# Kernel tuning notes

Measured on AMD Instinct MI355X. Metric: run time of the kernel, lower is better.

## Reference

```python
import jax, jax.numpy as jnp
import numpy as np

N = 100000
IN_DIM = 128
OUT_DIM = 128
E = 3200000


def setup_inputs() -> dict:
    key = jax.random.key(0)
    k1, k2, k3, k4, k5 = jax.random.split(key, 5)
    x = jax.random.normal(k1, (N, IN_DIM), dtype=jnp.float32)
    src = jax.random.randint(k2, (E,), 0, N)
    dst = jax.random.randint(k3, (E,), 0, N)
    edge_index = jnp.stack([src, dst], axis=0)  # (2, E) int
    # Linear(2*in_dim, out_dim): torch stores weight as (out, in)
    bound = 1.0 / np.sqrt(2 * IN_DIM)
    W = jax.random.uniform(k4, (OUT_DIM, 2 * IN_DIM), minval=-bound, maxval=bound, dtype=jnp.float32)
    b = jax.random.uniform(k5, (OUT_DIM,), minval=-bound, maxval=bound, dtype=jnp.float32)
    return {"x": x, "edge_index": edge_index, "W": W, "b": b}


def reference(x, edge_index, W, b):
    # x: (N, d), edge_index: (2, E)
    n = x.shape[0]
    src, dst = edge_index[0], edge_index[1]
    # scatter-add of source features into target buckets (mean aggregation)
    agg = jax.ops.segment_sum(x[src], dst, num_segments=n)          # (N, d)
    count = jax.ops.segment_sum(jnp.ones((src.shape[0],), x.dtype), dst, num_segments=n)
    count = jnp.maximum(count, 1.0)[:, None]                         # (N, 1)
    neigh_mean = agg / count
    combined = jnp.concatenate([x, neigh_mean], axis=1)              # (N, 2d)
    return combined @ W.T + b
```

## Files before the change

### kernel.cpp

```cpp
#include <hip/hip_runtime.h>

typedef unsigned int u32;
typedef unsigned short u16;
typedef unsigned char u8;
typedef _Float16 half8 __attribute__((ext_vector_type(8)));
typedef float f32x4 __attribute__((ext_vector_type(4)));
typedef float f32x2 __attribute__((ext_vector_type(2)));

__global__ __launch_bounds__(256) void pre_k(const float* __restrict__ x, u16* __restrict__ xh,
                                             u32* __restrict__ xq,
                                             const float* __restrict__ W, u16* __restrict__ wh,
                                             const int* __restrict__ dst, int E,
                                             u32* __restrict__ bktTotal, int N, int nbkt,
                                             int nba, int nbx) {
  int b = blockIdx.x, tid = threadIdx.x;
  if (b < nba) {
    __shared__ u32 h[512];
    for (int t = tid; t < 512; t += 256) h[t] = 0u;
    __syncthreads();
    int base = b * 8192;
    for (int it = 0; it < 32; it++) {
      int i = base + it * 256 + tid;
      if (i < E) atomicAdd(&h[(u32)dst[i] >> 8], 1u);
    }
    __syncthreads();
    for (int t = tid; t < nbkt; t += 256) {
      u32 c = h[t];
      if (c) atomicAdd(&bktTotal[t], c);
    }
  } else if (b < nba + nbx) {
    int i = (b - nba) * 256 + tid;
    if (i < N * 32) {
      const float4 v = *(const float4*)(x + (size_t)i * 4);
      u32 p0 = __builtin_bit_cast(u32, __builtin_amdgcn_cvt_pkrtz(v.x, v.y));
      u32 p1 = __builtin_bit_cast(u32, __builtin_amdgcn_cvt_pkrtz(v.z, v.w));
      *(uint2*)(xh + (size_t)i * 4) = uint2{p0, p1};
      u32 q = 0;
      q = __builtin_amdgcn_cvt_pk_fp8_f32(v.x, v.y, q, false);
      q = __builtin_amdgcn_cvt_pk_fp8_f32(v.z, v.w, q, true);
      xq[i] = q;
    }
  } else {
    int i = (b - nba - nbx) * 256 + tid;
    if (i < 8192) {
      const float4 v = *(const float4*)(W + (size_t)i * 4);
      u32 p0 = __builtin_bit_cast(u32, __builtin_amdgcn_cvt_pkrtz(v.x, v.y));
      u32 p1 = __builtin_bit_cast(u32, __builtin_amdgcn_cvt_pkrtz(v.z, v.w));
      *(uint2*)(wh + (size_t)i * 4) = uint2{p0, p1};
    }
  }
}

__global__ __launch_bounds__(512) void bscan_k(const u32* __restrict__ bktTotal, int nbkt,
                                               int E, int N, u32* __restrict__ start,
                                               u32* __restrict__ cursor, u32* __restrict__ offsets) {
  __shared__ u32 s[512];
  int t = threadIdx.x;
  u32 v = (t < nbkt) ? bktTotal[t] : 0u;
  s[t] = v;
  __syncthreads();
  for (int off = 1; off < 512; off <<= 1) {
    u32 x = (t >= off) ? s[t - off] : 0u;
    __syncthreads();
    s[t] += x;
    __syncthreads();
  }
  u32 excl = s[t] - v;
  if (t < nbkt) { start[t] = excl; cursor[t] = excl; }
  if (t == nbkt - 1) start[nbkt] = excl + v;
  if (t == 0) offsets[N] = (u32)E;
}

__global__ __launch_bounds__(256) void part_k(const int* __restrict__ src, const int* __restrict__ dst,
                                              int E, u32* __restrict__ cursor,
                                              u32* __restrict__ packed, int nbkt) {
  __shared__ u32 h[512];
  for (int t = threadIdx.x; t < 512; t += 256) h[t] = 0u;
  __syncthreads();
  int base = blockIdx.x * 8192;
  for (int it = 0; it < 32; it++) {
    int i = base + it * 256 + threadIdx.x;
    if (i < E) atomicAdd(&h[(u32)dst[i] >> 8], 1u);
  }
  __syncthreads();
  for (int t = threadIdx.x; t < nbkt; t += 256) {
    u32 c = h[t];
    h[t] = c ? atomicAdd(&cursor[t], c) : 0u;
  }
  __syncthreads();
  for (int it = 0; it < 32; it++) {
    int i = base + it * 256 + threadIdx.x;
    if (i < E) {
      u32 d = (u32)dst[i];
      u32 pos = atomicAdd(&h[d >> 8], 1u);
      packed[pos] = (u32)src[i] | ((d & 255u) << 24);
    }
  }
}

__global__ __launch_bounds__(256) void bucket_k(const u32* __restrict__ packed,
                                                const u32* __restrict__ start, int N,
                                                u32* __restrict__ offsets, int* __restrict__ ssrc,
                                                u8* __restrict__ nodeperm) {
  __shared__ u32 cnt[256];
  __shared__ u32 scn[256];
  __shared__ u32 cur[256];
  int b = blockIdx.x, t = threadIdx.x;
  u32 lo = start[b], hi = start[b + 1];
  cnt[t] = 0u;
  __syncthreads();
  for (u32 j = lo + t; j < hi; j += 256) atomicAdd(&cnt[packed[j] >> 24], 1u);
  __syncthreads();
  u32 v = cnt[t];
  scn[t] = v;
  __syncthreads();
  for (int off = 1; off < 256; off <<= 1) {
    u32 x = (t >= off) ? scn[t - off] : 0u;
    __syncthreads();
    scn[t] += x;
    __syncthreads();
  }
  u32 base = lo + scn[t] - v;
  int node = b * 256 + t;
  if (node < N) offsets[node] = base;
  cur[t] = base;
  __syncthreads();
  for (u32 j = lo + t; j < hi; j += 256) {
    u32 w = packed[j];
    u32 pos = atomicAdd(&cur[w >> 24], 1u);
    ssrc[pos] = (int)(w & 0xFFFFFFu);
  }
  {
    int g = t >> 5, l = t & 31;
    u32 mykey = cnt[t] * 256u + (u32)l;
    const u32* cg = &cnt[g * 32];
    u32 rank = 0;
#pragma unroll 8
    for (int l2 = 0; l2 < 32; l2++) {
      u32 k2 = cg[l2] * 256u + (u32)l2;
      rank += (k2 < mykey) ? 1u : 0u;
    }
    nodeperm[(size_t)b * 256 + g * 32 + rank] = (u8)l;
  }
}

#define DECV(vv, A0, A1, A2, A3) { f32x2 p;                              \
    p = __builtin_amdgcn_cvt_pk_f32_fp8((vv).x, false); A0 += p;         \
    p = __builtin_amdgcn_cvt_pk_f32_fp8((vv).x, true);  A1 += p;         \
    p = __builtin_amdgcn_cvt_pk_f32_fp8((vv).y, false); A2 += p;         \
    p = __builtin_amdgcn_cvt_pk_f32_fp8((vv).y, true);  A3 += p; }

__global__ __launch_bounds__(256) void fuse_k(const int* __restrict__ ssrc,
                                              const u32* __restrict__ offsets,
                                              const u32* __restrict__ xq,
                                              const u16* __restrict__ xh,
                                              const u16* __restrict__ wh,
                                              const float* __restrict__ bias,
                                              const u8* __restrict__ nodeperm,
                                              float* __restrict__ out, int N) {
  __shared__ u16 mlds[32][136];
  int wv = threadIdx.x >> 6, lane = threadIdx.x & 63;
  int sub = lane >> 4, cl = lane & 15;
  int nbase = blockIdx.x * 32;

  for (int r = 0; r < 2; r++) {
    int ln = nodeperm[(size_t)nbase + r * 16 + wv * 4 + sub];
    int node = nbase + ln;
    f32x2 A0{0.f,0.f}, A1{0.f,0.f}, A2{0.f,0.f}, A3{0.f,0.f};
    u32 deg = 0;
    if (node < N) {
      u32 s0 = offsets[node], s1 = offsets[node + 1];
      deg = s1 - s0;
      u32 j = s0;
      u32 nq = deg >> 2;
      if (nq) {
        uint4 iA = *(const uint4*)(ssrc + j);
        for (u32 q = 1; q < nq; q++) {
          uint4 iN = *(const uint4*)(ssrc + j + 4);
          uint2 v0 = *(const uint2*)(xq + ((size_t)iA.x << 5) + (cl << 1));
          uint2 v1 = *(const uint2*)(xq + ((size_t)iA.y << 5) + (cl << 1));
          uint2 v2 = *(const uint2*)(xq + ((size_t)iA.z << 5) + (cl << 1));
          uint2 v3 = *(const uint2*)(xq + ((size_t)iA.w << 5) + (cl << 1));
          DECV(v0, A0, A1, A2, A3) DECV(v1, A0, A1, A2, A3)
          DECV(v2, A0, A1, A2, A3) DECV(v3, A0, A1, A2, A3)
          iA = iN; j += 4;
        }
        {
          uint2 v0 = *(const uint2*)(xq + ((size_t)iA.x << 5) + (cl << 1));
          uint2 v1 = *(const uint2*)(xq + ((size_t)iA.y << 5) + (cl << 1));
          uint2 v2 = *(const uint2*)(xq + ((size_t)iA.z << 5) + (cl << 1));
          uint2 v3 = *(const uint2*)(xq + ((size_t)iA.w << 5) + (cl << 1));
          DECV(v0, A0, A1, A2, A3) DECV(v1, A0, A1, A2, A3)
          DECV(v2, A0, A1, A2, A3) DECV(v3, A0, A1, A2, A3)
          j += 4;
        }
      }
      for (; j < s1; j++) {
        int e = ssrc[j];
        uint2 v = *(const uint2*)(xq + ((size_t)e << 5) + (cl << 1));
        DECV(v, A0, A1, A2, A3)
      }
    }
    float inv = 1.0f / (float)(deg ? deg : 1u);
    u32 o0 = __builtin_bit_cast(u32, __builtin_amdgcn_cvt_pkrtz(A0.x * inv, A0.y * inv));
    u32 o1 = __builtin_bit_cast(u32, __builtin_amdgcn_cvt_pkrtz(A1.x * inv, A1.y * inv));
    u32 o2 = __builtin_bit_cast(u32, __builtin_amdgcn_cvt_pkrtz(A2.x * inv, A2.y * inv));
    u32 o3 = __builtin_bit_cast(u32, __builtin_amdgcn_cvt_pkrtz(A3.x * inv, A3.y * inv));
    *(uint4*)&mlds[ln][cl * 8] = uint4{o0, o1, o2, o3};
  }
  __syncthreads();

  int la = lane & 15, lb = lane >> 4;
  int strip = wv & 1, ch = wv >> 1;
  int rbase = nbase + strip * 16;
  half8 a[8];
  const u16* ab = xh + ((size_t)(rbase + la) << 7) + lb * 8;
#pragma unroll
  for (int kb = 0; kb < 4; kb++) a[kb] = *(const half8*)(ab + kb * 32);
#pragma unroll
  for (int kb = 0; kb < 4; kb++)
    a[4 + kb] = *(const half8*)(&mlds[strip * 16 + la][kb * 32 + lb * 8]);

#pragma unroll
  for (int c = 0; c < 4; c++) {
    int ct = ch * 4 + c;
    f32x4 acc = { 0.f, 0.f, 0.f, 0.f };
    const u16* bbase = wh + ((size_t)(ct * 16 + la) << 8) + lb * 8;
#pragma unroll
    for (int kb = 0; kb < 8; kb++) {
      half8 b = *(const half8*)(bbase + kb * 32);
      acc = __builtin_amdgcn_mfma_f32_16x16x32_f16(a[kb], b, acc, 0, 0, 0);
    }
    float bc = bias[ct * 16 + la];
#pragma unroll
    for (int jj = 0; jj < 4; jj++) {
      int rr = rbase + lb * 4 + jj;
      if (rr < N) out[((size_t)rr << 7) + ct * 16 + la] = acc[jj] + bc;
    }
  }
}

extern "C" void kernel_launch(void* const* d_in, const int* in_sizes, int n_in,
                              void* d_out, int out_size, void* d_ws, size_t ws_size,
                              hipStream_t stream) {
  const float* x    = (const float*)d_in[0];
  const int*   ei   = (const int*)d_in[1];
  const float* W    = (const float*)d_in[2];
  const float* bias = (const float*)d_in[3];
  const int N = in_sizes[0] / 128;
  const int E = in_sizes[1] / 2;
  const int nbkt = (N + 255) >> 8;
  const int* src = ei;
  const int* dst = ei + E;
  float* out = (float*)d_out;

  u32* packed   = (u32*)d_out;
  u32* bktTotal = packed + E;
  u32* start    = bktTotal + nbkt;
  u32* cursor   = start + nbkt + 1;

  char* ws = (char*)d_ws;
  u32* offsets = (u32*)ws;
  size_t off = ((size_t)(N + 1) * 4 + 255) & ~(size_t)255;
  int* ssrc = (int*)(ws + off);
  off += (size_t)E * 4;
  off = (off + 255) & ~(size_t)255;
  u16* xh = (u16*)(ws + off);
  off += (size_t)N * 128 * 2;
  off = (off + 255) & ~(size_t)255;
  u32* xq = (u32*)(ws + off);
  off += (size_t)N * 128;
  off = (off + 255) & ~(size_t)255;
  u16* wh = (u16*)(ws + off);
  off += (size_t)128 * 256 * 2;
  off = (off + 255) & ~(size_t)255;
  u8* nodeperm = (u8*)(ws + off);

  const int nbx = (N * 32 + 255) / 256;
  const int nba = (E + 8191) / 8192;
  hipMemsetAsync(bktTotal, 0, (size_t)nbkt * 4, stream);
  pre_k<<<nba + nbx + 32, 256, 0, stream>>>(x, xh, xq, W, wh, dst, E, bktTotal, N, nbkt, nba, nbx);
  bscan_k<<<1, 512, 0, stream>>>(bktTotal, nbkt, E, N, start, cursor, offsets);
  part_k<<<nba, 256, 0, stream>>>(src, dst, E, cursor, packed, nbkt);
  bucket_k<<<nbkt, 256, 0, stream>>>(packed, start, N, offsets, ssrc, nodeperm);
  fuse_k<<<(N + 31) / 32, 256, 0, stream>>>(ssrc, offsets, xq, xh, wh, bias, nodeperm, out, N);
}
```

Before: 208.1 us.

## Stage block edge indices in LDS and double-buffer neighbor gathers

Each block now cooperatively loads its contiguous range of sorted source indices (up to a fixed capacity) into shared memory, and per-node loops read indices from LDS instead of global memory. The gather loop is restructured to keep two groups of four neighbor-row loads in flight, consuming one while the next is issued. This aims to hide gather latency and remove the dependent global index loads from the critical path. It costs extra LDS, a block-wide barrier, and more registers, which may reduce occupancy.

```diff
diff --git a/kernel.cpp b/kernel.cpp
--- a/kernel.cpp
+++ b/kernel.cpp
@@ -6,6 +6,8 @@
 typedef _Float16 half8 __attribute__((ext_vector_type(8)));
 typedef float f32x4 __attribute__((ext_vector_type(4)));
 typedef float f32x2 __attribute__((ext_vector_type(2)));
+
+#define CAP 1536
 
 __global__ __launch_bounds__(256) void pre_k(const float* __restrict__ x, u16* __restrict__ xh,
                                              u32* __restrict__ xq,
@@ -144,11 +146,24 @@
   }
 }
 
-#define DECV(vv, A0, A1, A2, A3) { f32x2 p;                              \
+#define DECV(vv) { f32x2 p;                                              \
     p = __builtin_amdgcn_cvt_pk_f32_fp8((vv).x, false); A0 += p;         \
     p = __builtin_amdgcn_cvt_pk_f32_fp8((vv).x, true);  A1 += p;         \
     p = __builtin_amdgcn_cvt_pk_f32_fp8((vv).y, false); A2 += p;         \
     p = __builtin_amdgcn_cvt_pk_f32_fp8((vv).y, true);  A3 += p; }
+
+#define LOADQ(V0, V1, V2, V3, I) { \
+    V0 = *(const uint2*)(xq + ((size_t)(I).x << 5) + (cl << 1)); \
+    V1 = *(const uint2*)(xq + ((size_t)(I).y << 5) + (cl << 1)); \
+    V2 = *(const uint2*)(xq + ((size_t)(I).z << 5) + (cl << 1)); \
+    V3 = *(const uint2*)(xq + ((size_t)(I).w << 5) + (cl << 1)); }
+
+#define CONSQ(V0, V1, V2, V3) { DECV(V0) DECV(V1) DECV(V2) DECV(V3) }
+
+#define IDX4(O, DST) { if (inl) { int o_ = (int)(O); \
+      DST.x = (u32)eidx[o_]; DST.y = (u32)eidx[o_ + 1]; \
+      DST.z = (u32)eidx[o_ + 2]; DST.w = (u32)eidx[o_ + 3]; } \
+    else DST = *(const uint4*)((const u32*)ssrc + S0 + (O)); }
 
 __global__ __launch_bounds__(256) void fuse_k(const int* __restrict__ ssrc,
                                               const u32* __restrict__ offsets,
@@ -158,10 +173,24 @@
                                               const float* __restrict__ bias,
                                               const u8* __restrict__ nodeperm,
                                               float* __restrict__ out, int N) {
+  __shared__ int eidx[CAP];
   __shared__ u16 mlds[32][136];
   int wv = threadIdx.x >> 6, lane = threadIdx.x & 63;
   int sub = lane >> 4, cl = lane & 15;
+  int tid = threadIdx.x;
   int nbase = blockIdx.x * 32;
+
+  u32 S0 = offsets[nbase];
+  u32 S1 = offsets[nbase + 32 <= N ? nbase + 32 : N];
+  int cntE = (int)(S1 - S0);
+  int stg = cntE < CAP ? cntE : CAP;
+  for (int i = tid * 4; i + 3 < stg; i += 1024)
+    *(uint4*)&eidx[i] = *(const uint4*)(ssrc + S0 + i);
+  {
+    int base4 = stg & ~3;
+    if (tid < (stg & 3)) eidx[base4 + tid] = ssrc[S0 + base4 + tid];
+  }
+  __syncthreads();
 
   for (int r = 0; r < 2; r++) {
     int ln = nodeperm[(size_t)nbase + r * 16 + wv * 4 + sub];
@@ -171,34 +200,54 @@
     if (node < N) {
       u32 s0 = offsets[node], s1 = offsets[node + 1];
       deg = s1 - s0;
-      u32 j = s0;
+      const bool inl = ((s1 - S0) <= (u32)CAP);
+      u32 lb0 = s0 - S0;
       u32 nq = deg >> 2;
-      if (nq) {
-        uint4 iA = *(const uint4*)(ssrc + j);
-        for (u32 q = 1; q < nq; q++) {
-          uint4 iN = *(const uint4*)(ssrc + j + 4);
-          uint2 v0 = *(const uint2*)(xq + ((size_t)iA.x << 5) + (cl << 1));
-          uint2 v1 = *(const uint2*)(xq + ((size_t)iA.y << 5) + (cl << 1));
-          uint2 v2 = *(const uint2*)(xq + ((size_t)iA.z << 5) + (cl << 1));
-          uint2 v3 = *(const uint2*)(xq + ((size_t)iA.w << 5) + (cl << 1));
-          DECV(v0, A0, A1, A2, A3) DECV(v1, A0, A1, A2, A3)
-          DECV(v2, A0, A1, A2, A3) DECV(v3, A0, A1, A2, A3)
-          iA = iN; j += 4;
+      uint2 vA0, vA1, vA2, vA3, vB0, vB1, vB2, vB3;
+      u32 j;
+      if (nq >= 2) {
+        uint4 iA, iB;
+        IDX4(lb0, iA)
+        IDX4(lb0 + 4, iB)
+        LOADQ(vA0, vA1, vA2, vA3, iA)
+        LOADQ(vB0, vB1, vB2, vB3, iB)
+        u32 q = 2;
+        for (; q + 1 < nq; q += 2) {
+          uint4 i1, i2;
+          IDX4(lb0 + q * 4, i1)
+          IDX4(lb0 + q * 4 + 4, i2)
+          CONSQ(vA0, vA1, vA2, vA3)
+          LOADQ(vA0, vA1, vA2, vA3, i1)
+          CONSQ(vB0, vB1, vB2, vB3)
+          LOADQ(vB0, vB1, vB2, vB3, i2)
         }
-        {
-          uint2 v0 = *(const uint2*)(xq + ((size_t)iA.x << 5) + (cl << 1));
-          uint2 v1 = *(const uint2*)(xq + ((size_t)iA.y << 5) + (cl << 1));
-          uint2 v2 = *(const uint2*)(xq + ((size_t)iA.z << 5) + (cl << 1));
-          uint2 v3 = *(const uint2*)(xq + ((size_t)iA.w << 5) + (cl << 1));
-          DECV(v0, A0, A1, A2, A3) DECV(v1, A0, A1, A2, A3)
-          DECV(v2, A0, A1, A2, A3) DECV(v3, A0, A1, A2, A3)
-          j += 4;
+        if (q < nq) {
+          uint4 i1;
+          IDX4(lb0 + q * 4, i1)
+          CONSQ(vA0, vA1, vA2, vA3)
+          LOADQ(vA0, vA1, vA2, vA3, i1)
+          CONSQ(vB0, vB1, vB2, vB3)
+          CONSQ(vA0, vA1, vA2, vA3)
+          q++;
+        } else {
+          CONSQ(vA0, vA1, vA2, vA3)
+          CONSQ(vB0, vB1, vB2, vB3)
         }
+        j = s0 + nq * 4u;
+      } else if (nq == 1) {
+        uint4 iA;
+        IDX4(lb0, iA)
+        LOADQ(vA0, vA1, vA2, vA3, iA)
+        CONSQ(vA0, vA1, vA2, vA3)
+        j = s0 + 4u;
+      } else {
+        j = s0;
       }
       for (; j < s1; j++) {
-        int e = ssrc[j];
+        u32 o = j - S0;
+        int e = inl ? eidx[o] : ssrc[j];
         uint2 v = *(const uint2*)(xq + ((size_t)e << 5) + (cl << 1));
-        DECV(v, A0, A1, A2, A3)
+        DECV(v)
       }
     }
     float inv = 1.0f / (float)(deg ? deg : 1u);
```

Measured after the change: 209.1 us. About the same (+0.5%).

## Fuse per-node bucket sort into gather kernel using 64-node buckets in LDS

Applied to the files above, without the earlier changes.

Drops the separate bucket_k pass. Edges are partitioned into 64-node buckets, and each fuse_k block sorts its bucket's edges by destination node in shared memory, in tiles of up to CAP entries, before gathering. This removes the global ssrc/offsets/nodeperm writes and reads and one kernel launch. It also enlarges the partition blocks and moves packed into the workspace. The cost is larger LDS use per block, which lowers occupancy, plus extra LDS sort work inside the gather kernel. Buckets with more edges than CAP fall back to a multi-tile path without degree-sorted scheduling.

```diff
diff --git a/kernel.cpp b/kernel.cpp
--- a/kernel.cpp
+++ b/kernel.cpp
@@ -6,6 +6,11 @@
 typedef _Float16 half8 __attribute__((ext_vector_type(8)));
 typedef float f32x4 __attribute__((ext_vector_type(4)));
 typedef float f32x2 __attribute__((ext_vector_type(2)));
+
+#define BK 64
+#define CAP 3072
+#define EB 32768
+#define HSZ 1568
 
 __global__ __launch_bounds__(256) void pre_k(const float* __restrict__ x, u16* __restrict__ xh,
                                              u32* __restrict__ xq,
@@ -15,13 +20,13 @@
                                              int nba, int nbx) {
   int b = blockIdx.x, tid = threadIdx.x;
   if (b < nba) {
-    __shared__ u32 h[512];
-    for (int t = tid; t < 512; t += 256) h[t] = 0u;
-    __syncthreads();
-    int base = b * 8192;
-    for (int it = 0; it < 32; it++) {
+    __shared__ u32 h[HSZ];
+    for (int t = tid; t < HSZ; t += 256) h[t] = 0u;
+    __syncthreads();
+    int base = b * EB;
+    for (int it = 0; it < EB / 256; it++) {
       int i = base + it * 256 + tid;
-      if (i < E) atomicAdd(&h[(u32)dst[i] >> 8], 1u);
+      if (i < E) atomicAdd(&h[(u32)dst[i] >> 6], 1u);
     }
     __syncthreads();
     for (int t = tid; t < nbkt; t += 256) {
@@ -51,36 +56,38 @@
   }
 }
 
-__global__ __launch_bounds__(512) void bscan_k(const u32* __restrict__ bktTotal, int nbkt,
-                                               int E, int N, u32* __restrict__ start,
-                                               u32* __restrict__ cursor, u32* __restrict__ offsets) {
-  __shared__ u32 s[512];
+__global__ __launch_bounds__(1024) void bscan_k(const u32* __restrict__ bktTotal, int nbkt,
+                                                u32* __restrict__ start, u32* __restrict__ cursor) {
+  __shared__ u32 s[1024];
   int t = threadIdx.x;
-  u32 v = (t < nbkt) ? bktTotal[t] : 0u;
-  s[t] = v;
-  __syncthreads();
-  for (int off = 1; off < 512; off <<= 1) {
+  int i0 = t * 2, i1 = t * 2 + 1;
+  u32 a = (i0 < nbkt) ? bktTotal[i0] : 0u;
+  u32 b = (i1 < nbkt) ? bktTotal[i1] : 0u;
+  u32 sum = a + b;
+  s[t] = sum;
+  __syncthreads();
+  for (int off = 1; off < 1024; off <<= 1) {
     u32 x = (t >= off) ? s[t - off] : 0u;
     __syncthreads();
     s[t] += x;
     __syncthreads();
   }
-  u32 excl = s[t] - v;
-  if (t < nbkt) { start[t] = excl; cursor[t] = excl; }
-  if (t == nbkt - 1) start[nbkt] = excl + v;
-  if (t == 0) offsets[N] = (u32)E;
+  u32 excl = s[t] - sum;
+  if (i0 < nbkt) { start[i0] = excl; cursor[i0] = excl; }
+  if (i1 < nbkt) { start[i1] = excl + a; cursor[i1] = excl + a; }
+  if (t == 1023) start[nbkt] = s[1023];
 }
 
 __global__ __launch_bounds__(256) void part_k(const int* __restrict__ src, const int* __restrict__ dst,
                                               int E, u32* __restrict__ cursor,
                                               u32* __restrict__ packed, int nbkt) {
-  __shared__ u32 h[512];
-  for (int t = threadIdx.x; t < 512; t += 256) h[t] = 0u;
-  __syncthreads();
-  int base = blockIdx.x * 8192;
-  for (int it = 0; it < 32; it++) {
+  __shared__ u32 h[HSZ];
+  for (int t = threadIdx.x; t < HSZ; t += 256) h[t] = 0u;
+  __syncthreads();
+  int base = blockIdx.x * EB;
+  for (int it = 0; it < EB / 256; it++) {
     int i = base + it * 256 + threadIdx.x;
-    if (i < E) atomicAdd(&h[(u32)dst[i] >> 8], 1u);
+    if (i < E) atomicAdd(&h[(u32)dst[i] >> 6], 1u);
   }
   __syncthreads();
   for (int t = threadIdx.x; t < nbkt; t += 256) {
@@ -88,142 +95,145 @@
     h[t] = c ? atomicAdd(&cursor[t], c) : 0u;
   }
   __syncthreads();
-  for (int it = 0; it < 32; it++) {
+  for (int it = 0; it < EB / 256; it++) {
     int i = base + it * 256 + threadIdx.x;
     if (i < E) {
       u32 d = (u32)dst[i];
-      u32 pos = atomicAdd(&h[d >> 8], 1u);
-      packed[pos] = (u32)src[i] | ((d & 255u) << 24);
-    }
-  }
-}
-
-__global__ __launch_bounds__(256) void bucket_k(const u32* __restrict__ packed,
-                                                const u32* __restrict__ start, int N,
-                                                u32* __restrict__ offsets, int* __restrict__ ssrc,
-                                                u8* __restrict__ nodeperm) {
-  __shared__ u32 cnt[256];
-  __shared__ u32 scn[256];
-  __shared__ u32 cur[256];
-  int b = blockIdx.x, t = threadIdx.x;
-  u32 lo = start[b], hi = start[b + 1];
-  cnt[t] = 0u;
-  __syncthreads();
-  for (u32 j = lo + t; j < hi; j += 256) atomicAdd(&cnt[packed[j] >> 24], 1u);
-  __syncthreads();
-  u32 v = cnt[t];
-  scn[t] = v;
-  __syncthreads();
-  for (int off = 1; off < 256; off <<= 1) {
-    u32 x = (t >= off) ? scn[t - off] : 0u;
-    __syncthreads();
-    scn[t] += x;
-    __syncthreads();
-  }
-  u32 base = lo + scn[t] - v;
-  int node = b * 256 + t;
-  if (node < N) offsets[node] = base;
-  cur[t] = base;
-  __syncthreads();
-  for (u32 j = lo + t; j < hi; j += 256) {
-    u32 w = packed[j];
-    u32 pos = atomicAdd(&cur[w >> 24], 1u);
-    ssrc[pos] = (int)(w & 0xFFFFFFu);
-  }
-  {
-    int g = t >> 5, l = t & 31;
-    u32 mykey = cnt[t] * 256u + (u32)l;
-    const u32* cg = &cnt[g * 32];
-    u32 rank = 0;
-#pragma unroll 8
-    for (int l2 = 0; l2 < 32; l2++) {
-      u32 k2 = cg[l2] * 256u + (u32)l2;
-      rank += (k2 < mykey) ? 1u : 0u;
-    }
-    nodeperm[(size_t)b * 256 + g * 32 + rank] = (u8)l;
-  }
-}
-
-#define DECV(vv, A0, A1, A2, A3) { f32x2 p;                              \
-    p = __builtin_amdgcn_cvt_pk_f32_fp8((vv).x, false); A0 += p;         \
-    p = __builtin_amdgcn_cvt_pk_f32_fp8((vv).x, true);  A1 += p;         \
-    p = __builtin_amdgcn_cvt_pk_f32_fp8((vv).y, false); A2 += p;         \
-    p = __builtin_amdgcn_cvt_pk_f32_fp8((vv).y, true);  A3 += p; }
-
-__global__ __launch_bounds__(256) void fuse_k(const int* __restrict__ ssrc,
-                                              const u32* __restrict__ offsets,
+      u32 pos = atomicAdd(&h[d >> 6], 1u);
+      packed[pos] = (u32)src[i] | ((d & 63u) << 24);
+    }
+  }
+}
+
+#define DECQ(vv, B0, B1, B2, B3) { f32x2 p;                              \
+    p = __builtin_amdgcn_cvt_pk_f32_fp8((vv).x, false); B0 += p;         \
+    p = __builtin_amdgcn_cvt_pk_f32_fp8((vv).x, true);  B1 += p;         \
+    p = __builtin_amdgcn_cvt_pk_f32_fp8((vv).y, false); B2 += p;         \
+    p = __builtin_amdgcn_cvt_pk_f32_fp8((vv).y, true);  B3 += p; }
+
+#define GATHER(LN, B0, B1, B2, B3, DG) {                                          \
+    u32 sb = o64[LN]; u32 c = c64[LN]; DG += c;                                   \
+    u32 nq = c >> 2;                                                              \
+    if (nq) {                                                                     \
+      const int* ep = &eidx[sb];                                                  \
+      uint4 iA; iA.x=(u32)ep[0]; iA.y=(u32)ep[1]; iA.z=(u32)ep[2]; iA.w=(u32)ep[3]; \
+      for (u32 qq = 1; qq < nq; qq++) {                                           \
+        const int* en = &eidx[sb + qq * 4u];                                      \
+        uint4 iN; iN.x=(u32)en[0]; iN.y=(u32)en[1]; iN.z=(u32)en[2]; iN.w=(u32)en[3]; \
+        uint2 v0 = *(const uint2*)(xq + ((size_t)iA.x << 5) + (cl << 1));         \
+        uint2 v1 = *(const uint2*)(xq + ((size_t)iA.y << 5) + (cl << 1));         \
+        uint2 v2 = *(const uint2*)(xq + ((size_t)iA.z << 5) + (cl << 1));         \
+        uint2 v3 = *(const uint2*)(xq + ((size_t)iA.w << 5) + (cl << 1));         \
+        DECQ(v0, B0, B1, B2, B3) DECQ(v1, B0, B1, B2, B3)                         \
+        DECQ(v2, B0, B1, B2, B3) DECQ(v3, B0, B1, B2, B3)                         \
+        iA = iN;                                                                  \
+      }                                                                           \
+      {                                                                           \
+        uint2 v0 = *(const uint2*)(xq + ((size_t)iA.x << 5) + (cl << 1));         \
+        uint2 v1 = *(const uint2*)(xq + ((size_t)iA.y << 5) + (cl << 1));         \
+        uint2 v2 = *(const uint2*)(xq + ((size_t)iA.z << 5) + (cl << 1));         \
+        uint2 v3 = *(const uint2*)(xq + ((size_t)iA.w << 5) + (cl << 1));         \
+        DECQ(v0, B0, B1, B2, B3) DECQ(v1, B0, B1, B2, B3)                         \
+        DECQ(v2, B0, B1, B2, B3) DECQ(v3, B0, B1, B2, B3)                         \
+      }                                                                           \
+    }                                                                             \
+    for (u32 j = nq * 4u; j < c; j++) {                                           \
+      u32 e = (u32)eidx[sb + j];                                                  \
+      uint2 v = *(const uint2*)(xq + ((size_t)e << 5) + (cl << 1));               \
+      DECQ(v, B0, B1, B2, B3)                                                     \
+    } }
+
+#define WRMEAN(LN, B0, B1, B2, B3, DG) {                                          \
+    float inv = 1.0f / (float)((DG) ? (DG) : 1u);                                 \
+    u32 q0 = __builtin_bit_cast(u32, __builtin_amdgcn_cvt_pkrtz(B0.x*inv, B0.y*inv)); \
+    u32 q1 = __builtin_bit_cast(u32, __builtin_amdgcn_cvt_pkrtz(B1.x*inv, B1.y*inv)); \
+    u32 q2 = __builtin_bit_cast(u32, __builtin_amdgcn_cvt_pkrtz(B2.x*inv, B2.y*inv)); \
+    u32 q3 = __builtin_bit_cast(u32, __builtin_amdgcn_cvt_pkrtz(B3.x*inv, B3.y*inv)); \
+    *(uint4*)&mlds[LN][cl * 8] = uint4{q0, q1, q2, q3}; }
+
+__global__ __launch_bounds__(256) void fuse_k(const u32* __restrict__ packed,
+                                              const u32* __restrict__ start,
                                               const u32* __restrict__ xq,
                                               const u16* __restrict__ xh,
                                               const u16* __restrict__ wh,
                                               const float* __restrict__ bias,
-                                              const u8* __restrict__ nodeperm,
                                               float* __restrict__ out, int N) {
-  __shared__ u16 mlds[32][136];
-  int wv = threadIdx.x >> 6, lane = threadIdx.x & 63;
+  __shared__ int eidx[CAP];
+  __shared__ u16 mlds[64][136];
+  __shared__ u32 c64[64], o64[64], cur64[64], perm[64];
+  int tid = threadIdx.x, wv = tid >> 6, lane = tid & 63;
   int sub = lane >> 4, cl = lane & 15;
-  int nbase = blockIdx.x * 32;
-
-  for (int r = 0; r < 2; r++) {
-    int ln = nodeperm[(size_t)nbase + r * 16 + wv * 4 + sub];
-    int node = nbase + ln;
-    f32x2 A0{0.f,0.f}, A1{0.f,0.f}, A2{0.f,0.f}, A3{0.f,0.f};
-    u32 deg = 0;
-    if (node < N) {
-      u32 s0 = offsets[node], s1 = offsets[node + 1];
-      deg = s1 - s0;
-      u32 j = s0;
-      u32 nq = deg >> 2;
-      if (nq) {
-        uint4 iA = *(const uint4*)(ssrc + j);
-        for (u32 q = 1; q < nq; q++) {
-          uint4 iN = *(const uint4*)(ssrc + j + 4);
-          uint2 v0 = *(const uint2*)(xq + ((size_t)iA.x << 5) + (cl << 1));
-          uint2 v1 = *(const uint2*)(xq + ((size_t)iA.y << 5) + (cl << 1));
-          uint2 v2 = *(const uint2*)(xq + ((size_t)iA.z << 5) + (cl << 1));
-          uint2 v3 = *(const uint2*)(xq + ((size_t)iA.w << 5) + (cl << 1));
-          DECV(v0, A0, A1, A2, A3) DECV(v1, A0, A1, A2, A3)
-          DECV(v2, A0, A1, A2, A3) DECV(v3, A0, A1, A2, A3)
-          iA = iN; j += 4;
-        }
-        {
-          uint2 v0 = *(const uint2*)(xq + ((size_t)iA.x << 5) + (cl << 1));
-          uint2 v1 = *(const uint2*)(xq + ((size_t)iA.y << 5) + (cl << 1));
-          uint2 v2 = *(const uint2*)(xq + ((size_t)iA.z << 5) + (cl << 1));
-          uint2 v3 = *(const uint2*)(xq + ((size_t)iA.w << 5) + (cl << 1));
-          DECV(v0, A0, A1, A2, A3) DECV(v1, A0, A1, A2, A3)
-          DECV(v2, A0, A1, A2, A3) DECV(v3, A0, A1, A2, A3)
-          j += 4;
-        }
+  int nbase = blockIdx.x * BK;
+  u32 lo = start[blockIdx.x], hi = start[blockIdx.x + 1];
+  u32 cnt = hi - lo;
+  int ntiles = (int)((cnt + (CAP - 1)) / CAP);
+  bool single = (ntiles <= 1);
+
+  f32x2 A00{0,0},A01{0,0},A02{0,0},A03{0,0};
+  f32x2 A10{0,0},A11{0,0},A12{0,0},A13{0,0};
+  f32x2 A20{0,0},A21{0,0},A22{0,0},A23{0,0};
+  f32x2 A30{0,0},A31{0,0},A32{0,0},A33{0,0};
+  u32 dg0 = 0, dg1 = 0, dg2 = 0, dg3 = 0;
+  int rb = wv * 4 + sub;
+  int ln0 = rb, ln1 = 16 + rb, ln2 = 32 + rb, ln3 = 48 + rb;
+
+  for (int t = 0; t < ntiles; t++) {
+    u32 tb = lo + (u32)t * CAP;
+    u32 rem = hi - tb;
+    int tsz = (int)(rem < (u32)CAP ? rem : (u32)CAP);
+    if (tid < 64) c64[tid] = 0u;
+    __syncthreads();
+    for (int i = tid; i < tsz; i += 256) atomicAdd(&c64[packed[tb + i] >> 24], 1u);
+    __syncthreads();
+    if (tid < 64) {
+      u32 mc = c64[tid];
+      u32 mykey = mc * 64u + (u32)tid;
+      u32 o = 0, rank = 0;
+      for (int l = 0; l < 64; l++) {
+        u32 cv = c64[l];
+        if (l < tid) o += cv;
+        u32 k2 = cv * 64u + (u32)l;
+        rank += (k2 < mykey) ? 1u : 0u;
       }
-      for (; j < s1; j++) {
-        int e = ssrc[j];
-        uint2 v = *(const uint2*)(xq + ((size_t)e << 5) + (cl << 1));
-        DECV(v, A0, A1, A2, A3)
-      }
-    }
-    float inv = 1.0f / (float)(deg ? deg : 1u);
-    u32 o0 = __builtin_bit_cast(u32, __builtin_amdgcn_cvt_pkrtz(A0.x * inv, A0.y * inv));
-    u32 o1 = __builtin_bit_cast(u32, __builtin_amdgcn_cvt_pkrtz(A1.x * inv, A1.y * inv));
-    u32 o2 = __builtin_bit_cast(u32, __builtin_amdgcn_cvt_pkrtz(A2.x * inv, A2.y * inv));
-    u32 o3 = __builtin_bit_cast(u32, __builtin_amdgcn_cvt_pkrtz(A3.x * inv, A3.y * inv));
-    *(uint4*)&mlds[ln][cl * 8] = uint4{o0, o1, o2, o3};
-  }
+      o64[tid] = o; cur64[tid] = o;
+      perm[rank] = (u32)tid;
+    }
+    __syncthreads();
+    for (int i = tid; i < tsz; i += 256) {
+      u32 w = packed[tb + i];
+      u32 pos = atomicAdd(&cur64[w >> 24], 1u);
+      eidx[pos] = (int)(w & 0xFFFFFFu);
+    }
+    __syncthreads();
+    if (single) {
+      ln0 = (int)perm[rb]; ln1 = (int)perm[16 + rb];
+      ln2 = (int)perm[32 + rb]; ln3 = (int)perm[48 + rb];
+    }
+    GATHER(ln0, A00, A01, A02, A03, dg0)
+    GATHER(ln1, A10, A11, A12, A13, dg1)
+    GATHER(ln2, A20, A21, A22, A23, dg2)
+    GATHER(ln3, A30, A31, A32, A33, dg3)
+    __syncthreads();
+  }
+
+  WRMEAN(ln0, A00, A01, A02, A03, dg0)
+  WRMEAN(ln1, A10, A11, A12, A13, dg1)
+  WRMEAN(ln2, A20, A21, A22, A23, dg2)
+  WRMEAN(ln3, A30, A31, A32, A33, dg3)
   __syncthreads();
 
   int la = lane & 15, lb = lane >> 4;
-  int strip = wv & 1, ch = wv >> 1;
-  int rbase = nbase + strip * 16;
+  int wbase = nbase + wv * 16;
   half8 a[8];
-  const u16* ab = xh + ((size_t)(rbase + la) << 7) + lb * 8;
+  const u16* ab = xh + ((size_t)(wbase + la) << 7) + lb * 8;
 #pragma unroll
   for (int kb = 0; kb < 4; kb++) a[kb] = *(const half8*)(ab + kb * 32);
 #pragma unroll
   for (int kb = 0; kb < 4; kb++)
-    a[4 + kb] = *(const half8*)(&mlds[strip * 16 + la][kb * 32 + lb * 8]);
-
-#pragma unroll
-  for (int c = 0; c < 4; c++) {
-    int ct = ch * 4 + c;
+    a[4 + kb] = *(const half8*)(&mlds[wv * 16 + la][kb * 32 + lb * 8]);
+
+#pragma unroll
+  for (int ct = 0; ct < 8; ct++) {
     f32x4 acc = { 0.f, 0.f, 0.f, 0.f };
     const u16* bbase = wh + ((size_t)(ct * 16 + la) << 8) + lb * 8;
 #pragma unroll
@@ -234,7 +244,7 @@
     float bc = bias[ct * 16 + la];
 #pragma unroll
     for (int jj = 0; jj < 4; jj++) {
-      int rr = rbase + lb * 4 + jj;
+      int rr = wbase + lb * 4 + jj;
       if (rr < N) out[((size_t)rr << 7) + ct * 16 + la] = acc[jj] + bc;
     }
   }
@@ -249,22 +259,18 @@
   const float* bias = (const float*)d_in[3];
   const int N = in_sizes[0] / 128;
   const int E = in_sizes[1] / 2;
-  const int nbkt = (N + 255) >> 8;
+  const int nbkt = (N + BK - 1) / BK;
   const int* src = ei;
   const int* dst = ei + E;
   float* out = (float*)d_out;
 
-  u32* packed   = (u32*)d_out;
-  u32* bktTotal = packed + E;
+  char* ws = (char*)d_ws;
+  u32* packed   = (u32*)ws;
+  size_t off = ((size_t)E * 4 + 255) & ~(size_t)255;
+  u32* bktTotal = (u32*)(ws + off);
   u32* start    = bktTotal + nbkt;
   u32* cursor   = start + nbkt + 1;
-
-  char* ws = (char*)d_ws;
-  u32* offsets = (u32*)ws;
-  size_t off = ((size_t)(N + 1) * 4 + 255) & ~(size_t)255;
-  int* ssrc = (int*)(ws + off);
-  off += (size_t)E * 4;
-  off = (off + 255) & ~(size_t)255;
+  off += ((size_t)(3 * nbkt + 1) * 4 + 255) & ~(size_t)255;
   u16* xh = (u16*)(ws + off);
   off += (size_t)N * 128 * 2;
   off = (off + 255) & ~(size_t)255;
@@ -272,16 +278,12 @@
   off += (size_t)N * 128;
   off = (off + 255) & ~(size_t)255;
   u16* wh = (u16*)(ws + off);
-  off += (size_t)128 * 256 * 2;
-  off = (off + 255) & ~(size_t)255;
-  u8* nodeperm = (u8*)(ws + off);
 
   const int nbx = (N * 32 + 255) / 256;
-  const int nba = (E + 8191) / 8192;
+  const int nba = (E + EB - 1) / EB;
   hipMemsetAsync(bktTotal, 0, (size_t)nbkt * 4, stream);
   pre_k<<<nba + nbx + 32, 256, 0, stream>>>(x, xh, xq, W, wh, dst, E, bktTotal, N, nbkt, nba, nbx);
-  bscan_k<<<1, 512, 0, stream>>>(bktTotal, nbkt, E, N, start, cursor, offsets);
+  bscan_k<<<1, 1024, 0, stream>>>(bktTotal, nbkt, start, cursor);
   part_k<<<nba, 256, 0, stream>>>(src, dst, E, cursor, packed, nbkt);
-  bucket_k<<<nbkt, 256, 0, stream>>>(packed, start, N, offsets, ssrc, nodeperm);
-  fuse_k<<<(N + 31) / 32, 256, 0, stream>>>(ssrc, offsets, xq, xh, wh, bias, nodeperm, out, N);
-}
+  fuse_k<<<nbkt, 256, 0, stream>>>(packed, start, xq, xh, wh, bias, out, N);
+}
```

After: 277.8 us. 33.5% more time.
